# Kernel tuning notes

Hardware: AMD Instinct MI355X
Metric: run time of the kernel (lower is better)

Reference implementation:

```python
import jax, jax.numpy as jnp
import numpy as np

N = 100_000   # nodes
E = 600_000   # edges
D = 128       # embed_dim
G = 1000      # graphs (batch ids)
L = 3         # num_layers


def setup_inputs() -> dict:
    key = jax.random.key(0)
    ks = jax.random.split(key, 12)
    s = 1.0 / np.sqrt(D)
    return {
        "x": jax.random.normal(ks[0], (N, D), jnp.float32),
        "edge_index": jax.random.randint(ks[1], (2, E), 0, N),
        "batch": jnp.sort(jax.random.randint(ks[2], (N,), 0, G)),
        "mask": jax.random.randint(ks[3], (N,), 0, 2),
        # stacked GCNConv weights/biases (in=hidden=out=D)
        "gcn_w": jax.random.normal(ks[4], (L, D, D), jnp.float32) * s,
        "gcn_b": jnp.zeros((L, D), jnp.float32),
        # MLP head: Linear(D,D) -> ReLU -> Linear(D,1)
        "lin1_w": jax.random.normal(ks[5], (D, D), jnp.float32) * s,
        "lin1_b": jnp.zeros((D,), jnp.float32),
        "lin2_w": jax.random.normal(ks[6], (D,), jnp.float32) * s,
        "lin2_b": jnp.zeros((), jnp.float32),
    }


def gcn_forward(x, src, dst, gcn_w, gcn_b):
    # symmetric gcn_norm with self-loops: deg[i] = 1 + in-degree(i)
    deg = jax.ops.segment_sum(jnp.ones((E,), x.dtype), dst, num_segments=N) + 1.0
    dinv = jax.lax.rsqrt(deg)
    enorm = dinv[src] * dinv[dst]          # [E] edge normalization
    self_norm = (dinv * dinv)[:, None]     # [N,1] self-loop normalization
    h = x
    for l in range(L):
        h = h @ gcn_w[l]                   # [N,D]
        h = (jax.ops.segment_sum(h[src] * enorm[:, None], dst, num_segments=N)
             + h * self_norm)
        h = h + gcn_b[l]
        if l < L - 1:
            h = jax.nn.relu(h)  # (dropout inactive at inference)
    return h


def reference(x, edge_index, batch, mask, gcn_w, gcn_b, lin1_w, lin1_b, lin2_w, lin2_b):
    src, dst = edge_index[0], edge_index[1]
    h = gcn_forward(x, src, dst, gcn_w, gcn_b)
    # MLP head -> per-node score [N]
    s = jax.nn.relu(h @ lin1_w + lin1_b) @ lin2_w + lin2_b
    s = jnp.where(mask == 0, jnp.float32(-1e9), s)
    # per-graph (segment) softmax — fused replacement for the unique/batch loop
    m = jax.ops.segment_max(s, batch, num_segments=G)
    e = jnp.exp(s - m[batch])
    z = jax.ops.segment_sum(e, batch, num_segments=G)
    return e / z[batch]
```

## Files before the change

### kernel.cpp

```cpp
#include <hip/hip_runtime.h>
#include <hip/hip_bf16.h>

typedef unsigned int u32;
typedef unsigned short u16;
typedef __attribute__((ext_vector_type(8))) short bf16x8;
typedef __attribute__((ext_vector_type(4))) float f32x4;

__device__ __forceinline__ float u16tof(u16 u){ return __uint_as_float(((u32)u) << 16); }
__device__ __forceinline__ float lo16(u32 v){ return __uint_as_float(v << 16); }
__device__ __forceinline__ float hi16(u32 v){ return __uint_as_float(v & 0xffff0000u); }
__device__ __forceinline__ u16 ftobf(float f){
  u32 b = __float_as_uint(f);
  return (u16)((b + 0x7FFFu + ((b >> 16) & 1u)) >> 16);
}
__device__ __forceinline__ u32 pack2(float a, float b){
  return (u32)ftobf(a) | ((u32)ftobf(b) << 16);
}
__device__ __forceinline__ float ldf(const void* p, int i, int isbf){
  return isbf ? u16tof(((const u16*)p)[i]) : ((const float*)p)[i];
}

__global__ __launch_bounds__(256) void k_prep(const void* __restrict__ gw, const void* __restrict__ l1w,
                                              const void* __restrict__ x, u16* __restrict__ Wf,
                                              u16* __restrict__ Hb, int L, int n8, int cvtB,
                                              const int* __restrict__ dst, int* __restrict__ cntbuf, int nE,
                                              int* __restrict__ flag){
  const int b = blockIdx.x;
  if (b >= L + 1 + cvtB){
    int e = (b - (L + 1 + cvtB)) * 256 + threadIdx.x;
    if (e < nE) atomicAdd(&cntbuf[dst[e]], 1);
    return;
  }
  __shared__ int cnt;
  if (threadIdx.x == 0) cnt = 0;
  __syncthreads();
  if (b <= L){
    int local = 0;
    for (int i = threadIdx.x; i < 4096; i += 256){
      u32 e = (((const u32*)gw)[i] >> 7) & 0xFFu;
      if (e >= 100u && e < 127u) local++;
    }
    atomicAdd(&cnt, local);
    __syncthreads();
    const int isbf = (cnt > 2048) ? 1 : 0;
    if (b == 0 && threadIdx.x == 0) *flag = isbf;

    const void* src = (b < L) ? gw : l1w;
    const int sbase = (b < L) ? b * 16384 : 0;
    u16* dstp = Wf + (size_t)b * 16384;
    for (int g = threadIdx.x; g < 2048; g += 256){
      const int t = g >> 8, ks = (g >> 6) & 3, lane = g & 63;
      const int n = t * 16 + (lane & 15);
      const int k0 = ks * 32 + ((lane >> 4) << 3);
      u16* d = dstp + (size_t)g * 8;
      #pragma unroll
      for (int j = 0; j < 8; ++j){
        d[j] = ftobf(ldf(src, sbase + (k0 + j) * 128 + n, isbf));
      }
    }
  } else {
    u32 e = (((const u32*)gw)[threadIdx.x] >> 7) & 0xFFu;
    atomicAdd(&cnt, (e >= 100u && e < 127u) ? 1 : 0);
    __syncthreads();
    if (cnt > 128) return;
    const int i = (b - (L + 1)) * 256 + threadIdx.x;
    if (i >= n8) return;
    const float4 a = ((const float4*)x)[i * 2];
    const float4 c = ((const float4*)x)[i * 2 + 1];
    u16* o = Hb + (size_t)i * 8;
    o[0] = ftobf(a.x); o[1] = ftobf(a.y); o[2] = ftobf(a.z); o[3] = ftobf(a.w);
    o[4] = ftobf(c.x); o[5] = ftobf(c.y); o[6] = ftobf(c.z); o[7] = ftobf(c.w);
  }
}

__global__ __launch_bounds__(256) void k_scan1(const int* __restrict__ cnt, int* __restrict__ boff,
                                               int* __restrict__ bsum, float* __restrict__ dinv, int n){
  __shared__ int sm[256];
  int t = threadIdx.x;
  int i = blockIdx.x * 256 + t;
  int v = (i < n) ? cnt[i] : 0;
  if (i < n) dinv[i] = rsqrtf((float)v + 1.0f);
  sm[t] = v; __syncthreads();
  for (int off = 1; off < 256; off <<= 1){
    int add = (t >= off) ? sm[t - off] : 0;
    __syncthreads();
    sm[t] += add;
    __syncthreads();
  }
  if (i < n) boff[i] = sm[t] - v;
  if (t == 255) bsum[blockIdx.x] = sm[255];
}

__global__ __launch_bounds__(256) void k_scan3(int* __restrict__ boff, const int* __restrict__ bsum, int nb,
                                               int n, int nE, const int* __restrict__ batch,
                                               int* __restrict__ goff, int G){
  __shared__ int sm[512];
  const int t = threadIdx.x;
  sm[t]       = (t < nb)       ? bsum[t]       : 0;
  sm[t + 256] = (t + 256 < nb) ? bsum[t + 256] : 0;
  __syncthreads();
  for (int off = 1; off < 512; off <<= 1){
    int v0 = (t >= off)       ? sm[t - off]       : 0;
    int v1 = (t + 256 >= off) ? sm[t + 256 - off] : 0;
    __syncthreads();
    sm[t] += v0; sm[t + 256] += v1;
    __syncthreads();
  }
  const int base = (blockIdx.x == 0) ? 0 : sm[blockIdx.x - 1];

  int i = blockIdx.x * 256 + t;
  if (i >= n) return;
  boff[i] += base;
  if (i == 0) boff[n] = nE;
  int b = batch[i];
  int prev = (i == 0) ? -1 : batch[i - 1];
  for (int g = prev + 1; g <= b; ++g) goff[g] = i;
  if (i == n - 1){
    for (int g = b + 1; g <= G; ++g) goff[g] = n;
  }
}

__global__ __launch_bounds__(256) void k_fill(const int* __restrict__ src, const int* __restrict__ dst,
                                              int* __restrict__ cnt, const int* __restrict__ boff,
                                              int* __restrict__ eid, int nE){
  int e = blockIdx.x * 256 + threadIdx.x;
  if (e >= nE) return;
  int d = dst[e];
  int old = atomicSub(&cnt[d], 1);
  eid[boff[d] + old - 1] = src[e];
}

__global__ __launch_bounds__(256) void k_mm(const void* __restrict__ X, const u16* __restrict__ Hb, int use_x,
                                            const u16* __restrict__ Wf, const float* __restrict__ dinv,
                                            u16* __restrict__ T, int n, const int* __restrict__ fl){
  __shared__ u16 smw[16384];
  const int isbf = *fl;
  const u16* A = (use_x && isbf) ? (const u16*)X : Hb;
  {
    const uint4* s = (const uint4*)Wf;
    uint4* d = (uint4*)smw;
    for (int i = threadIdx.x; i < 2048; i += 256) d[i] = s[i];
  }
  __syncthreads();

  const int wave = threadIdx.x >> 6, lane = threadIdx.x & 63;
  const int m0 = blockIdx.x * 64 + wave * 16;
  int arow = m0 + (lane & 15); if (arow > n - 1) arow = n - 1;
  const u16* aptr = A + (size_t)arow * 128 + ((lane >> 4) << 3);

  f32x4 acc[8];
  #pragma unroll
  for (int t = 0; t < 8; ++t) acc[t] = (f32x4){0.f, 0.f, 0.f, 0.f};

  #pragma unroll
  for (int ks = 0; ks < 4; ++ks){
    const bf16x8 a = *(const bf16x8*)(aptr + ks * 32);
    #pragma unroll
    for (int t = 0; t < 8; ++t){
      const bf16x8 b = *(const bf16x8*)(smw + (size_t)(((t * 4 + ks) * 64 + lane) * 8));
      acc[t] = __builtin_amdgcn_mfma_f32_16x16x32_bf16(a, b, acc[t], 0, 0, 0);
    }
  }
  __syncthreads();

  const int quad = lane >> 4, col0 = lane & 15;
  float dv[4];
  #pragma unroll
  for (int r = 0; r < 4; ++r){
    const int row = m0 + quad * 4 + r;
    dv[r] = (row < n) ? dinv[row] : 0.f;
  }
  u16* my = smw + wave * 2112;
  #pragma unroll
  for (int t = 0; t < 8; ++t){
    #pragma unroll
    for (int r = 0; r < 4; ++r){
      my[(quad * 4 + r) * 132 + t * 16 + col0] = ftobf(acc[t][r] * dv[r]);
    }
  }
  #pragma unroll
  for (int i = 0; i < 4; ++i){
    const int row = i * 4 + (lane >> 4);
    const int grow = m0 + row;
    const int c8 = (lane & 15) * 8;
    if (grow < n){
      const u16* s = &my[row * 132 + c8];
      uint2 lo = *(const uint2*)(s);
      uint2 hi = *(const uint2*)(s + 4);
      *(uint4*)&T[(size_t)grow * 128 + c8] = make_uint4(lo.x, lo.y, hi.x, hi.y);
    }
  }
}

__global__ __launch_bounds__(256) void k_mmhead(const u16* __restrict__ Hb, const u16* __restrict__ Wf,
                                                const void* __restrict__ b1, const void* __restrict__ w2,
                                                const void* __restrict__ b2, const int* __restrict__ mask,
                                                float* __restrict__ s, int n, const int* __restrict__ fl){
  __shared__ u16 smw[16384];
  const int isbf = *fl;
  {
    const uint4* sp = (const uint4*)Wf;
    uint4* d = (uint4*)smw;
    for (int i = threadIdx.x; i < 2048; i += 256) d[i] = sp[i];
  }
  __syncthreads();

  const int wave = threadIdx.x >> 6, lane = threadIdx.x & 63;
  const int m0 = blockIdx.x * 64 + wave * 16;
  int arow = m0 + (lane & 15); if (arow > n - 1) arow = n - 1;
  const u16* aptr = Hb + (size_t)arow * 128 + ((lane >> 4) << 3);

  f32x4 acc[8];
  #pragma unroll
  for (int t = 0; t < 8; ++t) acc[t] = (f32x4){0.f, 0.f, 0.f, 0.f};

  #pragma unroll
  for (int ks = 0; ks < 4; ++ks){
    const bf16x8 a = *(const bf16x8*)(aptr + ks * 32);
    #pragma unroll
    for (int t = 0; t < 8; ++t){
      const bf16x8 b = *(const bf16x8*)(smw + (size_t)(((t * 4 + ks) * 64 + lane) * 8));
      acc[t] = __builtin_amdgcn_mfma_f32_16x16x32_bf16(a, b, acc[t], 0, 0, 0);
    }
  }

  const int quad = lane >> 4, col0 = lane & 15;
  float rs0 = 0.f, rs1 = 0.f, rs2 = 0.f, rs3 = 0.f;
  #pragma unroll
  for (int t = 0; t < 8; ++t){
    const int col = t * 16 + col0;
    const float bv = ldf(b1, col, isbf);
    const float wv = ldf(w2, col, isbf);
    rs0 = fmaf(fmaxf(acc[t][0] + bv, 0.f), wv, rs0);
    rs1 = fmaf(fmaxf(acc[t][1] + bv, 0.f), wv, rs1);
    rs2 = fmaf(fmaxf(acc[t][2] + bv, 0.f), wv, rs2);
    rs3 = fmaf(fmaxf(acc[t][3] + bv, 0.f), wv, rs3);
  }
  #pragma unroll
  for (int k = 1; k < 16; k <<= 1){
    rs0 += __shfl_xor(rs0, k);
    rs1 += __shfl_xor(rs1, k);
    rs2 += __shfl_xor(rs2, k);
    rs3 += __shfl_xor(rs3, k);
  }
  if (col0 < 4){
    const int row = m0 + quad * 4 + col0;
    if (row < n){
      float sc = (col0 == 0 ? rs0 : col0 == 1 ? rs1 : col0 == 2 ? rs2 : rs3) + ldf(b2, 0, isbf);
      if (mask[row] == 0) sc = -1e9f;
      s[row] = sc;
    }
  }
}

__global__ __launch_bounds__(256) void k_gather(const u16* __restrict__ T, const int* __restrict__ boff,
                                                const int* __restrict__ eid, const float* __restrict__ dinv,
                                                const void* __restrict__ bias, int layer,
                                                u16* __restrict__ H, int n, int relu,
                                                const int* __restrict__ fl){
  const int wave = threadIdx.x >> 6, lane = threadIdx.x & 63;
  const int sub = lane >> 4, l16 = lane & 15;
  const int node = blockIdx.x * 16 + wave * 4 + sub;
  if (node >= n) return;
  const int isbf = *fl;
  const float di = dinv[node];
  const uint4 sv = ((const uint4*)(T + (size_t)node * 128))[l16];
  float acc0 = lo16(sv.x), acc1 = hi16(sv.x), acc2 = lo16(sv.y), acc3 = hi16(sv.y);
  float acc4 = lo16(sv.z), acc5 = hi16(sv.z), acc6 = lo16(sv.w), acc7 = hi16(sv.w);

  int j = boff[node];
  const int b1 = boff[node + 1];
  for (; j + 4 <= b1; j += 4){
    const int s0 = eid[j], s1 = eid[j + 1], s2 = eid[j + 2], s3 = eid[j + 3];
    const uint4 v0 = ((const uint4*)(T + (size_t)s0 * 128))[l16];
    const uint4 v1 = ((const uint4*)(T + (size_t)s1 * 128))[l16];
    const uint4 v2 = ((const uint4*)(T + (size_t)s2 * 128))[l16];
    const uint4 v3 = ((const uint4*)(T + (size_t)s3 * 128))[l16];
    acc0 += (lo16(v0.x) + lo16(v1.x)) + (lo16(v2.x) + lo16(v3.x));
    acc1 += (hi16(v0.x) + hi16(v1.x)) + (hi16(v2.x) + hi16(v3.x));
    acc2 += (lo16(v0.y) + lo16(v1.y)) + (lo16(v2.y) + lo16(v3.y));
    acc3 += (hi16(v0.y) + hi16(v1.y)) + (hi16(v2.y) + hi16(v3.y));
    acc4 += (lo16(v0.z) + lo16(v1.z)) + (lo16(v2.z) + lo16(v3.z));
    acc5 += (hi16(v0.z) + hi16(v1.z)) + (hi16(v2.z) + hi16(v3.z));
    acc6 += (lo16(v0.w) + lo16(v1.w)) + (lo16(v2.w) + lo16(v3.w));
    acc7 += (hi16(v0.w) + hi16(v1.w)) + (hi16(v2.w) + hi16(v3.w));
  }
  for (; j < b1; ++j){
    const uint4 v = ((const uint4*)(T + (size_t)eid[j] * 128))[l16];
    acc0 += lo16(v.x); acc1 += hi16(v.x);
    acc2 += lo16(v.y); acc3 += hi16(v.y);
    acc4 += lo16(v.z); acc5 += hi16(v.z);
    acc6 += lo16(v.w); acc7 += hi16(v.w);
  }
  const int bb = layer * 128 + l16 * 8;
  float h0 = fmaf(acc0, di, ldf(bias, bb + 0, isbf));
  float h1 = fmaf(acc1, di, ldf(bias, bb + 1, isbf));
  float h2 = fmaf(acc2, di, ldf(bias, bb + 2, isbf));
  float h3 = fmaf(acc3, di, ldf(bias, bb + 3, isbf));
  float h4 = fmaf(acc4, di, ldf(bias, bb + 4, isbf));
  float h5 = fmaf(acc5, di, ldf(bias, bb + 5, isbf));
  float h6 = fmaf(acc6, di, ldf(bias, bb + 6, isbf));
  float h7 = fmaf(acc7, di, ldf(bias, bb + 7, isbf));
  if (relu){
    h0 = fmaxf(h0, 0.f); h1 = fmaxf(h1, 0.f); h2 = fmaxf(h2, 0.f); h3 = fmaxf(h3, 0.f);
    h4 = fmaxf(h4, 0.f); h5 = fmaxf(h5, 0.f); h6 = fmaxf(h6, 0.f); h7 = fmaxf(h7, 0.f);
  }
  uint4 o;
  o.x = pack2(h0, h1); o.y = pack2(h2, h3); o.z = pack2(h4, h5); o.w = pack2(h6, h7);
  ((uint4*)(H + (size_t)node * 128))[l16] = o;
}

__global__ __launch_bounds__(256) void k_gsm(const float* __restrict__ s, const int* __restrict__ goff,
                                             void* __restrict__ out, int G, const int* __restrict__ fl){
  const int g = blockIdx.x * 4 + (threadIdx.x >> 6);
  if (g >= G) return;
  const int lane = threadIdx.x & 63;
  const int i0 = goff[g], i1 = goff[g + 1];
  if (i0 >= i1) return;
  float m = -3.4e38f;
  for (int j = i0 + lane; j < i1; j += 64) m = fmaxf(m, s[j]);
  #pragma unroll
  for (int k = 32; k; k >>= 1) m = fmaxf(m, __shfl_xor(m, k));
  float zz = 0.f;
  for (int j = i0 + lane; j < i1; j += 64) zz += expf(s[j] - m);
  #pragma unroll
  for (int k = 32; k; k >>= 1) zz += __shfl_xor(zz, k);
  const float rz = 1.f / zz;
  const int isbf = *fl;
  for (int j = i0 + lane; j < i1; j += 64){
    const float v = expf(s[j] - m) * rz;
    if (isbf) ((u16*)out)[j] = ftobf(v);
    else      ((float*)out)[j] = v;
  }
}

extern "C" void kernel_launch(void* const* d_in, const int* in_sizes, int n_in,
                              void* d_out, int out_size, void* d_ws, size_t ws_size,
                              hipStream_t stream){
  const void* x    = d_in[0];
  const int* ei    = (const int*)d_in[1];
  const int* batch = (const int*)d_in[2];
  const int* mask  = (const int*)d_in[3];
  const void* gw   = d_in[4];
  const void* gb   = d_in[5];
  const void* l1w  = d_in[6];
  const void* l1b  = d_in[7];
  const void* l2w  = d_in[8];
  const void* l2b  = d_in[9];

  const int N = in_sizes[2];
  const int E = in_sizes[1] / 2;
  const int D = 128;
  const int L = in_sizes[4] / (D * D);
  const int G = 1000;

  char* p = (char*)d_ws;
  u16*  Hb    = (u16*)p;   p += (size_t)N * D * sizeof(u16);
  u16*  Tb    = (u16*)p;   p += (size_t)N * D * sizeof(u16);
  u16*  Wf    = (u16*)p;   p += (size_t)(L + 1) * D * D * sizeof(u16);
  float* dinv = (float*)p; p += (size_t)N * sizeof(float);
  float* sbuf = (float*)p; p += (size_t)N * sizeof(float);
  int*  cnt   = (int*)p;   p += (size_t)N * sizeof(int);
  int*  boff  = (int*)p;   p += (size_t)(N + 1) * sizeof(int);
  int*  bsum  = (int*)p;   p += 1024 * sizeof(int);
  int*  eid   = (int*)p;   p += (size_t)E * sizeof(int);
  int*  goff  = (int*)p;   p += (size_t)(G + 1) * sizeof(int);
  int*  flag  = (int*)p;   p += 256;

  const int* src  = ei;
  const int* dstp = ei + E;

  hipMemsetAsync(cnt, 0, (size_t)N * sizeof(int), stream);

  const int nb1 = (N + 255) / 256;
  const int mmg = (N + 63) / 64;
  const int ndg = (N + 15) / 16;
  const int n8  = N * D / 8;
  const int cvtB = (n8 + 255) / 256;
  const int cntB = (E + 255) / 256;

  k_prep<<<(L + 1) + cvtB + cntB, 256, 0, stream>>>(gw, l1w, x, Wf, Hb, L, n8, cvtB, dstp, cnt, E, flag);
  k_scan1<<<nb1, 256, 0, stream>>>(cnt, boff, bsum, dinv, N);
  k_scan3<<<nb1, 256, 0, stream>>>(boff, bsum, nb1, N, E, batch, goff, G);
  k_fill<<<cntB, 256, 0, stream>>>(src, dstp, cnt, boff, eid, E);

  for (int l = 0; l < L; ++l){
    k_mm<<<mmg, 256, 0, stream>>>(x, Hb, (l == 0) ? 1 : 0, Wf + (size_t)l * D * D, dinv, Tb, N, flag);
    k_gather<<<ndg, 256, 0, stream>>>(Tb, boff, eid, dinv, gb, l, Hb, N, (l < L - 1) ? 1 : 0, flag);
  }
  k_mmhead<<<mmg, 256, 0, stream>>>(Hb, Wf + (size_t)L * D * D, l1b, l2w, l2b, mask, sbuf, N, flag);
  k_gsm<<<(G + 3) / 4, 256, 0, stream>>>(sbuf, goff, d_out, G, flag);
}
```

Baseline: 368.3 us.

## Build CSR with two-level bucketed counting sort instead of global atomics

Replaces the global per-node atomic degree count, two-pass scan and atomic fill with a two-level counting sort. Edges are first histogrammed into 512-node buckets in shared memory, then scattered into a bucket-ordered temporary buffer, then sorted locally per bucket with shared-memory atomics. The same local pass also produces dinv and the row offsets. This removes the memset and the heavily contended global atomics, and folds the graph-offset computation into the prep kernel. The cost is an extra temporary edge array and a single-block scan kernel.

```diff
diff --git a/kernel.cpp b/kernel.cpp
--- a/kernel.cpp
+++ b/kernel.cpp
@@ -22,35 +22,53 @@
 
 __global__ __launch_bounds__(256) void k_prep(const void* __restrict__ gw, const void* __restrict__ l1w,
                                               const void* __restrict__ x, u16* __restrict__ Wf,
-                                              u16* __restrict__ Hb, int L, int n8, int cvtB,
-                                              const int* __restrict__ dst, int* __restrict__ cntbuf, int nE,
-                                              int* __restrict__ flag){
+                                              u16* __restrict__ Hb, int L, int n8, int cvtB, int goffB,
+                                              const int* __restrict__ batch, int* __restrict__ goff,
+                                              int N, int G,
+                                              const int* __restrict__ dst, int* __restrict__ hist,
+                                              int nE, int chunk, int* __restrict__ flag){
+  __shared__ int sh[256];
   const int b = blockIdx.x;
+  const int t = threadIdx.x;
+  const int histStart = L + 1 + cvtB + goffB;
+
+  if (b >= histStart){
+    sh[t] = 0; __syncthreads();
+    const int blk = b - histStart;
+    const int e0 = blk * chunk, e1 = min(e0 + chunk, nE);
+    for (int e = e0 + t; e < e1; e += 256) atomicAdd(&sh[dst[e] >> 9], 1);
+    __syncthreads();
+    hist[blk * 256 + t] = sh[t];
+    return;
+  }
   if (b >= L + 1 + cvtB){
-    int e = (b - (L + 1 + cvtB)) * 256 + threadIdx.x;
-    if (e < nE) atomicAdd(&cntbuf[dst[e]], 1);
+    const int i = (b - (L + 1 + cvtB)) * 256 + t;
+    if (i >= N) return;
+    const int bt = batch[i];
+    const int prev = (i == 0) ? -1 : batch[i - 1];
+    for (int g = prev + 1; g <= bt; ++g) goff[g] = i;
+    if (i == N - 1){ for (int g = bt + 1; g <= G; ++g) goff[g] = N; }
     return;
   }
-  __shared__ int cnt;
-  if (threadIdx.x == 0) cnt = 0;
+  if (t == 0) sh[0] = 0;
   __syncthreads();
   if (b <= L){
     int local = 0;
-    for (int i = threadIdx.x; i < 4096; i += 256){
+    for (int i = t; i < 4096; i += 256){
       u32 e = (((const u32*)gw)[i] >> 7) & 0xFFu;
       if (e >= 100u && e < 127u) local++;
     }
-    atomicAdd(&cnt, local);
-    __syncthreads();
-    const int isbf = (cnt > 2048) ? 1 : 0;
-    if (b == 0 && threadIdx.x == 0) *flag = isbf;
+    atomicAdd(&sh[0], local);
+    __syncthreads();
+    const int isbf = (sh[0] > 2048) ? 1 : 0;
+    if (b == 0 && t == 0) *flag = isbf;
 
     const void* src = (b < L) ? gw : l1w;
     const int sbase = (b < L) ? b * 16384 : 0;
     u16* dstp = Wf + (size_t)b * 16384;
-    for (int g = threadIdx.x; g < 2048; g += 256){
-      const int t = g >> 8, ks = (g >> 6) & 3, lane = g & 63;
-      const int n = t * 16 + (lane & 15);
+    for (int g = t; g < 2048; g += 256){
+      const int tt = g >> 8, ks = (g >> 6) & 3, lane = g & 63;
+      const int n = tt * 16 + (lane & 15);
       const int k0 = ks * 32 + ((lane >> 4) << 3);
       u16* d = dstp + (size_t)g * 8;
       #pragma unroll
@@ -59,11 +77,11 @@
       }
     }
   } else {
-    u32 e = (((const u32*)gw)[threadIdx.x] >> 7) & 0xFFu;
-    atomicAdd(&cnt, (e >= 100u && e < 127u) ? 1 : 0);
-    __syncthreads();
-    if (cnt > 128) return;
-    const int i = (b - (L + 1)) * 256 + threadIdx.x;
+    u32 e = (((const u32*)gw)[t] >> 7) & 0xFFu;
+    atomicAdd(&sh[0], (e >= 100u && e < 127u) ? 1 : 0);
+    __syncthreads();
+    if (sh[0] > 128) return;
+    const int i = (b - (L + 1)) * 256 + t;
     if (i >= n8) return;
     const float4 a = ((const float4*)x)[i * 2];
     const float4 c = ((const float4*)x)[i * 2 + 1];
@@ -73,61 +91,78 @@
   }
 }
 
-__global__ __launch_bounds__(256) void k_scan1(const int* __restrict__ cnt, int* __restrict__ boff,
-                                               int* __restrict__ bsum, float* __restrict__ dinv, int n){
+__global__ __launch_bounds__(256) void k_hscan(int* __restrict__ hist, int* __restrict__ bb, int nE){
+  const int t = threadIdx.x;
+  int run = 0;
+  for (int j = 0; j < 256; ++j){
+    const int v = hist[j * 256 + t];
+    hist[j * 256 + t] = run;
+    run += v;
+  }
   __shared__ int sm[256];
-  int t = threadIdx.x;
-  int i = blockIdx.x * 256 + t;
-  int v = (i < n) ? cnt[i] : 0;
-  if (i < n) dinv[i] = rsqrtf((float)v + 1.0f);
-  sm[t] = v; __syncthreads();
+  sm[t] = run; __syncthreads();
   for (int off = 1; off < 256; off <<= 1){
-    int add = (t >= off) ? sm[t - off] : 0;
-    __syncthreads();
-    sm[t] += add;
-    __syncthreads();
-  }
-  if (i < n) boff[i] = sm[t] - v;
-  if (t == 255) bsum[blockIdx.x] = sm[255];
-}
-
-__global__ __launch_bounds__(256) void k_scan3(int* __restrict__ boff, const int* __restrict__ bsum, int nb,
-                                               int n, int nE, const int* __restrict__ batch,
-                                               int* __restrict__ goff, int G){
-  __shared__ int sm[512];
-  const int t = threadIdx.x;
-  sm[t]       = (t < nb)       ? bsum[t]       : 0;
-  sm[t + 256] = (t + 256 < nb) ? bsum[t + 256] : 0;
+    int a = (t >= off) ? sm[t - off] : 0;
+    __syncthreads();
+    sm[t] += a;
+    __syncthreads();
+  }
+  bb[t] = sm[t] - run;
+  if (t == 255) bb[256] = nE;
+}
+
+__global__ __launch_bounds__(256) void k_scatter(const int* __restrict__ src, const int* __restrict__ dst,
+                                                 const int* __restrict__ hist, const int* __restrict__ bb,
+                                                 int2* __restrict__ tmpe, int nE, int chunk){
+  __shared__ int base[256];
+  const int blk = blockIdx.x, t = threadIdx.x;
+  base[t] = bb[t] + hist[blk * 256 + t];
+  __syncthreads();
+  const int e0 = blk * chunk, e1 = min(e0 + chunk, nE);
+  for (int e = e0 + t; e < e1; e += 256){
+    const int d = dst[e];
+    const int pos = atomicAdd(&base[d >> 9], 1);
+    tmpe[pos] = make_int2(src[e], d);
+  }
+}
+
+__global__ __launch_bounds__(256) void k_local(const int2* __restrict__ tmpe, const int* __restrict__ bb,
+                                               int* __restrict__ boff, int* __restrict__ eid,
+                                               float* __restrict__ dinv, int N, int nE, int nbkt){
+  __shared__ int hcnt[512];
+  __shared__ int hoff[512];
+  const int b = blockIdx.x, t = threadIdx.x;
+  const int n0 = b << 9;
+  const int n1 = min(n0 + 512, N);
+  const int nn = n1 - n0;
+  const int e0 = bb[b], e1 = bb[b + 1];
+  hcnt[t] = 0; hcnt[t + 256] = 0;
+  __syncthreads();
+  for (int e = e0 + t; e < e1; e += 256) atomicAdd(&hcnt[tmpe[e].y - n0], 1);
+  __syncthreads();
+  const int v0 = hcnt[t], v1 = hcnt[t + 256];
+  hoff[t] = v0; hoff[t + 256] = v1;
   __syncthreads();
   for (int off = 1; off < 512; off <<= 1){
-    int v0 = (t >= off)       ? sm[t - off]       : 0;
-    int v1 = (t + 256 >= off) ? sm[t + 256 - off] : 0;
-    __syncthreads();
-    sm[t] += v0; sm[t + 256] += v1;
-    __syncthreads();
-  }
-  const int base = (blockIdx.x == 0) ? 0 : sm[blockIdx.x - 1];
-
-  int i = blockIdx.x * 256 + t;
-  if (i >= n) return;
-  boff[i] += base;
-  if (i == 0) boff[n] = nE;
-  int b = batch[i];
-  int prev = (i == 0) ? -1 : batch[i - 1];
-  for (int g = prev + 1; g <= b; ++g) goff[g] = i;
-  if (i == n - 1){
-    for (int g = b + 1; g <= G; ++g) goff[g] = n;
-  }
-}
-
-__global__ __launch_bounds__(256) void k_fill(const int* __restrict__ src, const int* __restrict__ dst,
-                                              int* __restrict__ cnt, const int* __restrict__ boff,
-                                              int* __restrict__ eid, int nE){
-  int e = blockIdx.x * 256 + threadIdx.x;
-  if (e >= nE) return;
-  int d = dst[e];
-  int old = atomicSub(&cnt[d], 1);
-  eid[boff[d] + old - 1] = src[e];
+    int a0 = (t >= off) ? hoff[t - off] : 0;
+    int a1 = (t + 256 >= off) ? hoff[t + 256 - off] : 0;
+    __syncthreads();
+    hoff[t] += a0; hoff[t + 256] += a1;
+    __syncthreads();
+  }
+  const int ex0 = hoff[t] - v0 + e0;
+  const int ex1 = hoff[t + 256] - v1 + e0;
+  if (t < nn){       boff[n0 + t] = ex0;        dinv[n0 + t] = rsqrtf((float)v0 + 1.0f); }
+  if (t + 256 < nn){ boff[n0 + t + 256] = ex1;  dinv[n0 + t + 256] = rsqrtf((float)v1 + 1.0f); }
+  if (b == nbkt - 1 && t == 0) boff[N] = nE;
+  __syncthreads();
+  hoff[t] = ex0; hoff[t + 256] = ex1;
+  __syncthreads();
+  for (int e = e0 + t; e < e1; e += 256){
+    const int2 pr = tmpe[e];
+    const int pos = atomicAdd(&hoff[pr.y - n0], 1);
+    eid[pos] = pr.x;
+  }
 }
 
 __global__ __launch_bounds__(256) void k_mm(const void* __restrict__ X, const u16* __restrict__ Hb, int use_x,
@@ -360,29 +395,30 @@
   u16*  Wf    = (u16*)p;   p += (size_t)(L + 1) * D * D * sizeof(u16);
   float* dinv = (float*)p; p += (size_t)N * sizeof(float);
   float* sbuf = (float*)p; p += (size_t)N * sizeof(float);
-  int*  cnt   = (int*)p;   p += (size_t)N * sizeof(int);
   int*  boff  = (int*)p;   p += (size_t)(N + 1) * sizeof(int);
-  int*  bsum  = (int*)p;   p += 1024 * sizeof(int);
   int*  eid   = (int*)p;   p += (size_t)E * sizeof(int);
   int*  goff  = (int*)p;   p += (size_t)(G + 1) * sizeof(int);
+  int*  hist  = (int*)p;   p += 256 * 256 * sizeof(int);
+  int*  bb    = (int*)p;   p += 260 * sizeof(int);
+  int2* tmpe  = (int2*)p;  p += (size_t)E * sizeof(int2);
   int*  flag  = (int*)p;   p += 256;
 
-  const int* src  = ei;
+  const int* srcp = ei;
   const int* dstp = ei + E;
 
-  hipMemsetAsync(cnt, 0, (size_t)N * sizeof(int), stream);
-
-  const int nb1 = (N + 255) / 256;
-  const int mmg = (N + 63) / 64;
-  const int ndg = (N + 15) / 16;
-  const int n8  = N * D / 8;
+  const int mmg  = (N + 63) / 64;
+  const int ndg  = (N + 15) / 16;
+  const int n8   = N * D / 8;
   const int cvtB = (n8 + 255) / 256;
-  const int cntB = (E + 255) / 256;
-
-  k_prep<<<(L + 1) + cvtB + cntB, 256, 0, stream>>>(gw, l1w, x, Wf, Hb, L, n8, cvtB, dstp, cnt, E, flag);
-  k_scan1<<<nb1, 256, 0, stream>>>(cnt, boff, bsum, dinv, N);
-  k_scan3<<<nb1, 256, 0, stream>>>(boff, bsum, nb1, N, E, batch, goff, G);
-  k_fill<<<cntB, 256, 0, stream>>>(src, dstp, cnt, boff, eid, E);
+  const int goffB = (N + 255) / 256;
+  const int chunk = (E + 255) / 256;
+  const int nbkt  = (N + 511) / 512;
+
+  k_prep<<<(L + 1) + cvtB + goffB + 256, 256, 0, stream>>>(gw, l1w, x, Wf, Hb, L, n8, cvtB, goffB,
+                                                           batch, goff, N, G, dstp, hist, E, chunk, flag);
+  k_hscan<<<1, 256, 0, stream>>>(hist, bb, E);
+  k_scatter<<<256, 256, 0, stream>>>(srcp, dstp, hist, bb, tmpe, E, chunk);
+  k_local<<<nbkt, 256, 0, stream>>>(tmpe, bb, boff, eid, dinv, N, E, nbkt);
 
   for (int l = 0; l < L; ++l){
     k_mm<<<mmg, 256, 0, stream>>>(x, Hb, (l == 0) ? 1 : 0, Wf + (size_t)l * D * D, dinv, Tb, N, flag);
```

New measurement: 335.3 us. 1.1x faster.
